# Kernel tuning notes

Measured on AMD Instinct MI355X. Metric: run time of the kernel, lower is better.

The kernel has to match this reference:

```python
import jax, jax.numpy as jnp
import numpy as np

N_NODES = 100000
N_EDGES = 1600000
F_IN = 256
F_HID = 128
BN_EPS = 1e-3


def setup_inputs() -> dict:
    key = jax.random.key(0)
    ks = jax.random.split(key, 10)
    x = jax.random.normal(ks[0], (N_NODES, F_IN), dtype=jnp.float32)
    edge_index = jax.random.randint(ks[1], (2, N_EDGES), 0, N_NODES, dtype=jnp.int64)
    edge_weight = jax.random.uniform(ks[2], (N_EDGES,), dtype=jnp.float32)
    # Layer 0: GCNConv 256 -> 128, Layer 1: GCNConv 128 -> 128
    W0 = jax.random.normal(ks[3], (F_IN, F_HID), dtype=jnp.float32) * (1.0 / np.sqrt(F_IN))
    b0 = jnp.zeros((F_HID,), dtype=jnp.float32)
    g0 = jnp.ones((F_HID,), dtype=jnp.float32)
    beta0 = jnp.zeros((F_HID,), dtype=jnp.float32)
    W1 = jax.random.normal(ks[4], (F_HID, F_HID), dtype=jnp.float32) * (1.0 / np.sqrt(F_HID))
    b1 = jnp.zeros((F_HID,), dtype=jnp.float32)
    g1 = jnp.ones((F_HID,), dtype=jnp.float32)
    beta1 = jnp.zeros((F_HID,), dtype=jnp.float32)
    return {"x": x, "edge_index": edge_index, "edge_weight": edge_weight,
            "W0": W0, "b0": b0, "g0": g0, "beta0": beta0,
            "W1": W1, "b1": b1, "g1": g1, "beta1": beta1}


def _gcn_conv(x, src, dst, ew, W, b):
    # PyG GCNConv: add self-loops (weight 1), symmetric normalization,
    # linear transform, scatter-aggregate over destination, then bias.
    h = x @ W                                            # [N, F_out]
    deg = jax.ops.segment_sum(ew, dst, num_segments=N_NODES) + 1.0  # +1 self-loop
    dinv = jnp.where(deg > 0, jax.lax.rsqrt(deg), 0.0)   # deg^{-1/2}
    norm = dinv[src] * ew * dinv[dst]                    # [E]
    agg = jax.ops.segment_sum(h[src] * norm[:, None], dst, num_segments=N_NODES)
    agg = agg + (dinv * dinv)[:, None] * h               # self-loop contribution
    return agg + b


def _batchnorm(x, gamma, beta):
    # training-mode BatchNorm1d math (batch stats, biased variance), eps=1e-3
    mu = jnp.mean(x, axis=0)
    var = jnp.mean(jnp.square(x - mu), axis=0)
    return (x - mu) * jax.lax.rsqrt(var + BN_EPS) * gamma + beta


def reference(x, edge_index, edge_weight, W0, b0, g0, beta0, W1, b1, g1, beta1):
    src, dst = edge_index[0], edge_index[1]
    # Layer 0: GCNConv -> BatchNorm -> ReLU -> Dropout(eval=identity)
    h = _gcn_conv(x, src, dst, edge_weight, W0, b0)
    h = jax.nn.relu(_batchnorm(h, g0, beta0))
    # Layer 1
    h = _gcn_conv(h, src, dst, edge_weight, W1, b1)
    h = jax.nn.relu(_batchnorm(h, g1, beta1))
    return h
```

## Files before the change

kernel.cpp:

```cpp
#include <hip/hip_runtime.h>
#include <stdint.h>

#define FIN 256
#define FHID 128
#define BN_EPS 1e-3f

#ifndef USE_GLL
#if defined(__has_builtin)
#if __has_builtin(__builtin_amdgcn_global_load_lds)
#define USE_GLL 1
#else
#define USE_GLL 0
#endif
#else
#define USE_GLL 0
#endif
#endif

typedef short bf16x8 __attribute__((ext_vector_type(8)));
typedef float f32x4 __attribute__((ext_vector_type(4)));

__device__ inline short f2bf(float f) {
    unsigned u = __float_as_uint(f);
    unsigned r = (u + 0x7FFFu + ((u >> 16) & 1u)) >> 16;
    return (short)r;
}
__device__ inline float bflo(unsigned v) { return __uint_as_float(v << 16); }
__device__ inline float bfhi(unsigned v) { return __uint_as_float(v & 0xFFFF0000u); }
__device__ inline float bf2f(short s) {
    return __uint_as_float(((unsigned)(unsigned short)s) << 16);
}

#define DEG_SCALE 131072.0f
#define DEG_INV   (1.0f / 131072.0f)

__global__ __launch_bounds__(256) void k_histprep(const int* __restrict__ ei, int E,
                                                  int HB, int CHUNKH, int nbuk,
                                                  unsigned* __restrict__ bcnt,
                                                  const float* __restrict__ W0,
                                                  const float* __restrict__ W1,
                                                  short* __restrict__ Wt0,
                                                  short* __restrict__ Wt1) {
    __shared__ unsigned hist[1024];
    if ((int)blockIdx.x < HB) {
        for (int i = threadIdx.x; i < nbuk; i += 256) hist[i] = 0;
        __syncthreads();
        const int e0 = blockIdx.x * CHUNKH;
        const int e1 = min(e0 + CHUNKH, E);
        for (int e = e0 + threadIdx.x; e < e1; e += 256)
            atomicAdd(&hist[ei[E + e] >> 7], 1u);
        __syncthreads();
        for (int k = threadIdx.x; k < nbuk; k += 256)
            bcnt[(size_t)blockIdx.x * nbuk + k] = hist[k];
    } else {
        int idx = ((int)blockIdx.x - HB) * 256 + threadIdx.x;
        if (idx < 32768) {
            int n = idx >> 8, k = idx & 255;
            Wt0[idx] = f2bf(W0[k * 128 + n]);
        } else {
            int j = idx - 32768;
            if (j < 16384) {
                int n = j >> 7, k = j & 127;
                Wt1[j] = f2bf(W1[k * 128 + n]);
            }
        }
    }
}

__device__ __forceinline__ void gemm0_body(int bid, float* xs,
                                           const float* __restrict__ X,
                                           const short* __restrict__ Wt,
                                           short* __restrict__ H, int nrows) {
    const int t = threadIdx.x;
    const int lane = t & 63;
    const int w = t >> 6;
    const int r0 = bid * 32;
    const int l15 = lane & 15;
    const int q = lane >> 4;

#pragma unroll
    for (int i = 0; i < 8; i++) {
        const int row = w * 8 + i;
        int grow = r0 + row; if (grow >= nrows) grow = nrows - 1;
        const char* gsrc = (const char*)(X + (size_t)grow * 256);
        const int swz = (row & 7) << 4;
#if USE_GLL
        __builtin_amdgcn_global_load_lds(gsrc + ((lane * 16) ^ swz),
                                         xs + row * 256, 16, 0, 0);
#else
        const float4 v = *reinterpret_cast<const float4*>(gsrc + ((lane * 16) ^ swz));
        *reinterpret_cast<float4*>((char*)xs + row * 1024 + lane * 16) = v;
#endif
    }
    __syncthreads();

    const int n0 = w * 32;
    const int swzr = (l15 & 7) << 4;

    f32x4 acc[2][2];
#pragma unroll
    for (int mf = 0; mf < 2; mf++)
#pragma unroll
        for (int nf = 0; nf < 2; nf++)
#pragma unroll
            for (int r = 0; r < 4; r++) acc[mf][nf][r] = 0.0f;

#pragma unroll
    for (int ks = 0; ks < 8; ks++) {
        const int cb = ks * 128 + q * 32;
        bf16x8 a[2];
#pragma unroll
        for (int mf = 0; mf < 2; mf++) {
            const char* rb = (const char*)xs + (size_t)(mf * 16 + l15) * 1024;
            const float4 u0 = *reinterpret_cast<const float4*>(rb + (cb ^ swzr));
            const float4 u1 = *reinterpret_cast<const float4*>(rb + ((cb + 16) ^ swzr));
            bf16x8 tt;
            tt[0] = f2bf(u0.x); tt[1] = f2bf(u0.y); tt[2] = f2bf(u0.z); tt[3] = f2bf(u0.w);
            tt[4] = f2bf(u1.x); tt[5] = f2bf(u1.y); tt[6] = f2bf(u1.z); tt[7] = f2bf(u1.w);
            a[mf] = tt;
        }
        const bf16x8 b0 = *reinterpret_cast<const bf16x8*>(
            Wt + (size_t)(n0 + l15) * 256 + ks * 32 + q * 8);
        const bf16x8 b1 = *reinterpret_cast<const bf16x8*>(
            Wt + (size_t)(n0 + 16 + l15) * 256 + ks * 32 + q * 8);
        acc[0][0] = __builtin_amdgcn_mfma_f32_16x16x32_bf16(a[0], b0, acc[0][0], 0, 0, 0);
        acc[1][0] = __builtin_amdgcn_mfma_f32_16x16x32_bf16(a[1], b0, acc[1][0], 0, 0, 0);
        acc[0][1] = __builtin_amdgcn_mfma_f32_16x16x32_bf16(a[0], b1, acc[0][1], 0, 0, 0);
        acc[1][1] = __builtin_amdgcn_mfma_f32_16x16x32_bf16(a[1], b1, acc[1][1], 0, 0, 0);
    }

#pragma unroll
    for (int mf = 0; mf < 2; mf++) {
        const int rbase = r0 + mf * 16 + (lane >> 4) * 4;
#pragma unroll
        for (int r = 0; r < 4; r++) {
            const int row = rbase + r;
            if (row < nrows) {
#pragma unroll
                for (int nf = 0; nf < 2; nf++)
                    H[(size_t)row * 128 + n0 + nf * 16 + l15] = f2bf(acc[mf][nf][r]);
            }
        }
    }
}

__global__ __launch_bounds__(256) void k_phaseCG(const int* __restrict__ ei,
                                                 const float* __restrict__ ew,
                                                 int E, int CHUNKC, int nbuk, int sub,
                                                 const unsigned* __restrict__ bcnt,
                                                 const unsigned* __restrict__ bbase,
                                                 int2* __restrict__ recs_mid,
                                                 int CBC,
                                                 const float* __restrict__ X,
                                                 const short* __restrict__ Wt,
                                                 short* __restrict__ H, int nrows) {
    __shared__ float xs[8192];
    if ((int)blockIdx.x < CBC) {
        unsigned* curs = (unsigned*)xs;
        const int b = blockIdx.x;
        for (int k = threadIdx.x; k < nbuk; k += 256)
            curs[k] = bbase[k] + bcnt[(size_t)(b * sub) * nbuk + k];
        __syncthreads();
        const int e0 = b * CHUNKC;
        const int e1 = min(e0 + CHUNKC, E);
        for (int base = e0; base < e1; base += 1024) {
            const int e = base + threadIdx.x * 4;
            if (e + 3 < e1) {
                const int4 s4 = *reinterpret_cast<const int4*>(ei + e);
                const int4 d4 = *reinterpret_cast<const int4*>(ei + E + e);
                const float4 w4 = *reinterpret_cast<const float4*>(ew + e);
                unsigned p0 = atomicAdd(&curs[d4.x >> 7], 1u);
                recs_mid[p0] = make_int2(s4.x | ((d4.x & 127) << 17), __float_as_int(w4.x));
                unsigned p1 = atomicAdd(&curs[d4.y >> 7], 1u);
                recs_mid[p1] = make_int2(s4.y | ((d4.y & 127) << 17), __float_as_int(w4.y));
                unsigned p2 = atomicAdd(&curs[d4.z >> 7], 1u);
                recs_mid[p2] = make_int2(s4.z | ((d4.z & 127) << 17), __float_as_int(w4.z));
                unsigned p3 = atomicAdd(&curs[d4.w >> 7], 1u);
                recs_mid[p3] = make_int2(s4.w | ((d4.w & 127) << 17), __float_as_int(w4.w));
            } else {
#pragma unroll
                for (int j = 0; j < 4; j++) {
                    const int ee = e + j;
                    if (ee < e1) {
                        int src = ei[ee];
                        int dst = ei[E + ee];
                        unsigned pos = atomicAdd(&curs[dst >> 7], 1u);
                        recs_mid[pos] = make_int2(src | ((dst & 127) << 17),
                                                  __float_as_int(ew[ee]));
                    }
                }
            }
        }
    } else {
        gemm0_body((int)blockIdx.x - CBC, xs, X, Wt, H, nrows);
    }
}

__global__ __launch_bounds__(256) void k_gemm1(const short* __restrict__ X,
                                               const short* __restrict__ Wt,
                                               const float* __restrict__ prm,
                                               short* __restrict__ H, int nrows) {
    __shared__ short xs[4096];
    const int t = threadIdx.x;
    const int lane = t & 63;
    const int w = t >> 6;
    const int r0 = blockIdx.x * 32;
    const int l15 = lane & 15;
    const int q = lane >> 4;

#pragma unroll
    for (int j = 0; j < 2; j++) {
        const int rbase = w * 8 + j * 4;
        const int row = rbase + q;
        int grow = r0 + row; if (grow >= nrows) grow = nrows - 1;
        const char* gsrc = (const char*)(X + (size_t)grow * 128);
        const int swz = (row & 7) << 4;
#if USE_GLL
        __builtin_amdgcn_global_load_lds(gsrc + (((lane & 15) * 16) ^ swz),
                                         xs + rbase * 128, 16, 0, 0);
#else
        const uint4 v = *reinterpret_cast<const uint4*>(gsrc + (((lane & 15) * 16) ^ swz));
        *reinterpret_cast<uint4*>((char*)xs + rbase * 256 + lane * 16) = v;
#endif
    }
    __syncthreads();

    const int n0 = w * 32;
    const int swzr = (l15 & 7) << 4;

    f32x4 acc[2][2];
#pragma unroll
    for (int mf = 0; mf < 2; mf++)
#pragma unroll
        for (int nf = 0; nf < 2; nf++)
#pragma unroll
            for (int r = 0; r < 4; r++) acc[mf][nf][r] = 0.0f;

#pragma unroll
    for (int ks = 0; ks < 4; ks++) {
        const int kb = ks * 32 + q * 8;
        const int cb = ks * 64 + q * 16;
        const float4 sc0 = *reinterpret_cast<const float4*>(prm + kb);
        const float4 sc1 = *reinterpret_cast<const float4*>(prm + kb + 4);
        const float4 sh0 = *reinterpret_cast<const float4*>(prm + 128 + kb);
        const float4 sh1 = *reinterpret_cast<const float4*>(prm + 128 + kb + 4);
        bf16x8 a[2];
#pragma unroll
        for (int mf = 0; mf < 2; mf++) {
            const char* rb = (const char*)xs + (size_t)(mf * 16 + l15) * 256;
            const bf16x8 ar = *reinterpret_cast<const bf16x8*>(rb + (cb ^ swzr));
            bf16x8 tt;
            tt[0] = f2bf(fmaxf(bf2f(ar[0]) * sc0.x + sh0.x, 0.f));
            tt[1] = f2bf(fmaxf(bf2f(ar[1]) * sc0.y + sh0.y, 0.f));
            tt[2] = f2bf(fmaxf(bf2f(ar[2]) * sc0.z + sh0.z, 0.f));
            tt[3] = f2bf(fmaxf(bf2f(ar[3]) * sc0.w + sh0.w, 0.f));
            tt[4] = f2bf(fmaxf(bf2f(ar[4]) * sc1.x + sh1.x, 0.f));
            tt[5] = f2bf(fmaxf(bf2f(ar[5]) * sc1.y + sh1.y, 0.f));
            tt[6] = f2bf(fmaxf(bf2f(ar[6]) * sc1.z + sh1.z, 0.f));
            tt[7] = f2bf(fmaxf(bf2f(ar[7]) * sc1.w + sh1.w, 0.f));
            a[mf] = tt;
        }
        const bf16x8 b0 = *reinterpret_cast<const bf16x8*>(
            Wt + (size_t)(n0 + l15) * 128 + kb);
        const bf16x8 b1 = *reinterpret_cast<const bf16x8*>(
            Wt + (size_t)(n0 + 16 + l15) * 128 + kb);
        acc[0][0] = __builtin_amdgcn_mfma_f32_16x16x32_bf16(a[0], b0, acc[0][0], 0, 0, 0);
        acc[1][0] = __builtin_amdgcn_mfma_f32_16x16x32_bf16(a[1], b0, acc[1][0], 0, 0, 0);
        acc[0][1] = __builtin_amdgcn_mfma_f32_16x16x32_bf16(a[0], b1, acc[0][1], 0, 0, 0);
        acc[1][1] = __builtin_amdgcn_mfma_f32_16x16x32_bf16(a[1], b1, acc[1][1], 0, 0, 0);
    }

#pragma unroll
    for (int mf = 0; mf < 2; mf++) {
        const int rbase = r0 + mf * 16 + (lane >> 4) * 4;
#pragma unroll
        for (int r = 0; r < 4; r++) {
            const int row = rbase + r;
            if (row < nrows) {
#pragma unroll
                for (int nf = 0; nf < 2; nf++)
                    H[(size_t)row * 128 + n0 + nf * 16 + l15] = f2bf(acc[mf][nf][r]);
            }
        }
    }
}

__global__ __launch_bounds__(256) void k_phaseB(unsigned* __restrict__ bcnt,
                                                unsigned* __restrict__ btotal,
                                                int HB, int nbuk) {
    __shared__ unsigned lds[256];
    const int k = blockIdx.x;
    const int t = threadIdx.x;
    unsigned v[4];
    unsigned s = 0;
#pragma unroll
    for (int i = 0; i < 4; i++) {
        int j = t * 4 + i;
        v[i] = (j < HB) ? bcnt[(size_t)j * nbuk + k] : 0;
        s += v[i];
    }
    lds[t] = s;
    __syncthreads();
    for (int off = 1; off < 256; off <<= 1) {
        unsigned add = (t >= off) ? lds[t - off] : 0;
        __syncthreads();
        lds[t] += add;
        __syncthreads();
    }
    unsigned run = lds[t] - s;
#pragma unroll
    for (int i = 0; i < 4; i++) {
        int j = t * 4 + i;
        if (j < HB) bcnt[(size_t)j * nbuk + k] = run;
        run += v[i];
    }
    if (t == 255) btotal[k] = lds[255];
}

__global__ __launch_bounds__(256) void k_bsum(const unsigned* __restrict__ btotal,
                                              unsigned* __restrict__ bbase,
                                              int nbuk, int E) {
    __shared__ unsigned lds[256];
    const int t = threadIdx.x;
    unsigned v[4];
    unsigned s = 0;
#pragma unroll
    for (int i = 0; i < 4; i++) {
        int j = t * 4 + i;
        v[i] = (j < nbuk) ? btotal[j] : 0;
        s += v[i];
    }
    lds[t] = s;
    __syncthreads();
    for (int off = 1; off < 256; off <<= 1) {
        unsigned add = (t >= off) ? lds[t - off] : 0;
        __syncthreads();
        lds[t] += add;
        __syncthreads();
    }
    unsigned run = lds[t] - s;
#pragma unroll
    for (int i = 0; i < 4; i++) {
        int j = t * 4 + i;
        if (j < nbuk) bbase[j] = run;
        run += v[i];
    }
    if (t == 255) bbase[nbuk] = (unsigned)E;
}

__global__ __launch_bounds__(256) void k_phaseD(const int2* __restrict__ recs_mid,
                                                const unsigned* __restrict__ bbase,
                                                float* __restrict__ dinv,
                                                int* __restrict__ rowptr,
                                                int2* __restrict__ recs,
                                                int n, int E) {
    __shared__ unsigned cnt[128], wsum[128], rank[128], sc[128], base[128];
    __shared__ float dloc[128];
    const int k = blockIdx.x;
    const int t = threadIdx.x;
    if (t < 128) { cnt[t] = 0; wsum[t] = 0; rank[t] = 0; }
    __syncthreads();
    const unsigned s0 = bbase[k], s1 = bbase[k + 1];
    for (unsigned i = s0 + t; i < s1; i += 256) {
        int2 r = recs_mid[i];
        int dl = (r.x >> 17) & 127;
        atomicAdd(&cnt[dl], 1u);
        atomicAdd(&wsum[dl], (unsigned)(__int_as_float(r.y) * DEG_SCALE));
    }
    __syncthreads();
    if (t < 128) sc[t] = cnt[t];
    __syncthreads();
    for (int off = 1; off < 128; off <<= 1) {
        unsigned add = (t < 128 && t >= off) ? sc[t - off] : 0;
        __syncthreads();
        if (t < 128) sc[t] += add;
        __syncthreads();
    }
    if (t < 128) {
        unsigned excl = sc[t] - cnt[t];
        base[t] = s0 + excl;
        int dst = k * 128 + t;
        if (dst < n) {
            float dg = (float)wsum[t] * DEG_INV + 1.0f;
            float dv = rsqrtf(dg);
            dloc[t] = dv;
            dinv[dst] = dv;
            rowptr[dst] = (int)(s0 + excl);
        }
    }
    if (k == 0 && t == 0) rowptr[n] = E;
    __syncthreads();
    for (unsigned i = s0 + t; i < s1; i += 256) {
        int2 r = recs_mid[i];
        int dl = (r.x >> 17) & 127;
        unsigned rr = atomicAdd(&rank[dl], 1u);
        float w2 = __int_as_float(r.y) * dloc[dl];
        recs[base[dl] + rr] = make_int2(r.x & 0x1FFFF, __float_as_int(w2));
    }
}

__global__ __launch_bounds__(256) void k_gather_stats(const short* __restrict__ h,
                                                      short* __restrict__ aggbf,
                                                      const int* __restrict__ rowptr,
                                                      const int2* __restrict__ recs,
                                                      const float* __restrict__ dinv,
                                                      const float* __restrict__ bias,
                                                      float* __restrict__ partial,
                                                      int n, int nstreams) {
    __shared__ float lsum[4][128], lsq[4][128];
    const int w = threadIdx.x >> 6;
    const int lane = threadIdx.x & 63;
    const int q3 = lane >> 4;
    const int f8 = (lane & 15) * 8;
    const float4 bv0 = *reinterpret_cast<const float4*>(bias + f8);
    const float4 bv1 = *reinterpret_cast<const float4*>(bias + f8 + 4);
    float s[8], qq[8];
#pragma unroll
    for (int j = 0; j < 8; j++) { s[j] = 0.f; qq[j] = 0.f; }

    for (int node = blockIdx.x * 16 + w * 4 + q3; node < n; node += nstreams) {
        float a[8];
#pragma unroll
        for (int j = 0; j < 8; j++) a[j] = 0.f;
        int e = rowptr[node];
        const int end = rowptr[node + 1];
        for (; e + 4 <= end; e += 4) {
            const int2 r0 = recs[e];
            const int2 r1 = recs[e + 1];
            const int2 r2 = recs[e + 2];
            const int2 r3 = recs[e + 3];
            const float d0 = dinv[r0.x];
            const float d1 = dinv[r1.x];
            const float d2 = dinv[r2.x];
            const float d3 = dinv[r3.x];
            const uint4 v0 = *reinterpret_cast<const uint4*>(h + (size_t)r0.x * 128 + f8);
            const uint4 v1 = *reinterpret_cast<const uint4*>(h + (size_t)r1.x * 128 + f8);
            const uint4 v2 = *reinterpret_cast<const uint4*>(h + (size_t)r2.x * 128 + f8);
            const uint4 v3 = *reinterpret_cast<const uint4*>(h + (size_t)r3.x * 128 + f8);
            const float w0 = __int_as_float(r0.y) * d0;
            const float w1 = __int_as_float(r1.y) * d1;
            const float w2 = __int_as_float(r2.y) * d2;
            const float w3 = __int_as_float(r3.y) * d3;
            a[0] += bflo(v0.x) * w0; a[1] += bfhi(v0.x) * w0;
            a[2] += bflo(v0.y) * w0; a[3] += bfhi(v0.y) * w0;
            a[4] += bflo(v0.z) * w0; a[5] += bfhi(v0.z) * w0;
            a[6] += bflo(v0.w) * w0; a[7] += bfhi(v0.w) * w0;
            a[0] += bflo(v1.x) * w1; a[1] += bfhi(v1.x) * w1;
            a[2] += bflo(v1.y) * w1; a[3] += bfhi(v1.y) * w1;
            a[4] += bflo(v1.z) * w1; a[5] += bfhi(v1.z) * w1;
            a[6] += bflo(v1.w) * w1; a[7] += bfhi(v1.w) * w1;
            a[0] += bflo(v2.x) * w2; a[1] += bfhi(v2.x) * w2;
            a[2] += bflo(v2.y) * w2; a[3] += bfhi(v2.y) * w2;
            a[4] += bflo(v2.z) * w2; a[5] += bfhi(v2.z) * w2;
            a[6] += bflo(v2.w) * w2; a[7] += bfhi(v2.w) * w2;
            a[0] += bflo(v3.x) * w3; a[1] += bfhi(v3.x) * w3;
            a[2] += bflo(v3.y) * w3; a[3] += bfhi(v3.y) * w3;
            a[4] += bflo(v3.z) * w3; a[5] += bfhi(v3.z) * w3;
            a[6] += bflo(v3.w) * w3; a[7] += bfhi(v3.w) * w3;
        }
        for (; e < end; e++) {
            const int2 r = recs[e];
            const float d = dinv[r.x];
            const uint4 v = *reinterpret_cast<const uint4*>(h + (size_t)r.x * 128 + f8);
            const float w0 = __int_as_float(r.y) * d;
            a[0] += bflo(v.x) * w0; a[1] += bfhi(v.x) * w0;
            a[2] += bflo(v.y) * w0; a[3] += bfhi(v.y) * w0;
            a[4] += bflo(v.z) * w0; a[5] += bfhi(v.z) * w0;
            a[6] += bflo(v.w) * w0; a[7] += bfhi(v.w) * w0;
        }
        const float di = dinv[node];
        const float sl = di * di;
        const uint4 hv = *reinterpret_cast<const uint4*>(h + (size_t)node * 128 + f8);
        float o[8];
        o[0] = a[0] + bflo(hv.x) * sl + bv0.x;
        o[1] = a[1] + bfhi(hv.x) * sl + bv0.y;
        o[2] = a[2] + bflo(hv.y) * sl + bv0.z;
        o[3] = a[3] + bfhi(hv.y) * sl + bv0.w;
        o[4] = a[4] + bflo(hv.z) * sl + bv1.x;
        o[5] = a[5] + bfhi(hv.z) * sl + bv1.y;
        o[6] = a[6] + bflo(hv.w) * sl + bv1.z;
        o[7] = a[7] + bfhi(hv.w) * sl + bv1.w;
        bf16x8 ob;
#pragma unroll
        for (int j = 0; j < 8; j++) ob[j] = f2bf(o[j]);
        *reinterpret_cast<bf16x8*>(aggbf + (size_t)node * 128 + f8) = ob;
#pragma unroll
        for (int j = 0; j < 8; j++) { s[j] += o[j]; qq[j] += o[j] * o[j]; }
    }

#pragma unroll
    for (int j = 0; j < 8; j++) {
        s[j] += __shfl_xor(s[j], 16);  s[j] += __shfl_xor(s[j], 32);
        qq[j] += __shfl_xor(qq[j], 16); qq[j] += __shfl_xor(qq[j], 32);
    }
    if (q3 == 0) {
        *reinterpret_cast<float4*>(&lsum[w][f8]) = make_float4(s[0], s[1], s[2], s[3]);
        *reinterpret_cast<float4*>(&lsum[w][f8 + 4]) = make_float4(s[4], s[5], s[6], s[7]);
        *reinterpret_cast<float4*>(&lsq[w][f8]) = make_float4(qq[0], qq[1], qq[2], qq[3]);
        *reinterpret_cast<float4*>(&lsq[w][f8 + 4]) = make_float4(qq[4], qq[5], qq[6], qq[7]);
    }
    __syncthreads();
    const int t = threadIdx.x;
    if (t < 128) {
        float ps = lsum[0][t] + lsum[1][t] + lsum[2][t] + lsum[3][t];
        float pq = lsq[0][t] + lsq[1][t] + lsq[2][t] + lsq[3][t];
        partial[(size_t)blockIdx.x * 256 + t] = ps;
        partial[(size_t)blockIdx.x * 256 + 128 + t] = pq;
    }
}

__global__ __launch_bounds__(256) void k_stats_bn(const float* __restrict__ partial,
                                                  const float* __restrict__ g,
                                                  const float* __restrict__ beta,
                                                  float* __restrict__ prm,
                                                  int nblk, int n) {
    __shared__ float wsm[4], wqm[4];
    const int f = blockIdx.x;
    const int t = threadIdx.x;
    const int per = nblk / 256;
    float s = 0.f, q = 0.f;
    for (int i = 0; i < per; i++) {
        int p = t * per + i;
        s += partial[(size_t)p * 256 + f];
        q += partial[(size_t)p * 256 + 128 + f];
    }
#pragma unroll
    for (int off = 1; off < 64; off <<= 1) {
        s += __shfl_xor(s, off);
        q += __shfl_xor(q, off);
    }
    if ((t & 63) == 0) { wsm[t >> 6] = s; wqm[t >> 6] = q; }
    __syncthreads();
    if (t == 0) {
        float S = wsm[0] + wsm[1] + wsm[2] + wsm[3];
        float Q = wqm[0] + wqm[1] + wqm[2] + wqm[3];
        float inv_n = 1.0f / (float)n;
        float mu = S * inv_n;
        float var = Q * inv_n - mu * mu;
        float sc = rsqrtf(var + BN_EPS) * g[f];
        prm[f] = sc;
        prm[128 + f] = beta[f] - mu * sc;
    }
}

__global__ __launch_bounds__(256) void k_bn_relu(const short* __restrict__ xbf,
                                                 float* __restrict__ y,
                                                 const float* __restrict__ prm, int n) {
    int idx = blockIdx.x * blockDim.x + threadIdx.x;
    const int total = n * 16;
    for (; idx < total; idx += gridDim.x * blockDim.x) {
        int node = idx >> 4;
        int f8 = (idx & 15) * 8;
        const uint4 v = *reinterpret_cast<const uint4*>(xbf + (size_t)node * 128 + f8);
        const float4 sc0 = *reinterpret_cast<const float4*>(prm + f8);
        const float4 sc1 = *reinterpret_cast<const float4*>(prm + f8 + 4);
        const float4 sh0 = *reinterpret_cast<const float4*>(prm + 128 + f8);
        const float4 sh1 = *reinterpret_cast<const float4*>(prm + 128 + f8 + 4);
        float4 o0, o1;
        o0.x = fmaxf(bflo(v.x) * sc0.x + sh0.x, 0.f);
        o0.y = fmaxf(bfhi(v.x) * sc0.y + sh0.y, 0.f);
        o0.z = fmaxf(bflo(v.y) * sc0.z + sh0.z, 0.f);
        o0.w = fmaxf(bfhi(v.y) * sc0.w + sh0.w, 0.f);
        o1.x = fmaxf(bflo(v.z) * sc1.x + sh1.x, 0.f);
        o1.y = fmaxf(bfhi(v.z) * sc1.y + sh1.y, 0.f);
        o1.z = fmaxf(bflo(v.w) * sc1.z + sh1.z, 0.f);
        o1.w = fmaxf(bfhi(v.w) * sc1.w + sh1.w, 0.f);
        float* yp = y + (size_t)node * 128 + f8;
        *reinterpret_cast<float4*>(yp) = o0;
        *reinterpret_cast<float4*>(yp + 4) = o1;
    }
}

extern "C" void kernel_launch(void* const* d_in, const int* in_sizes, int n_in,
                              void* d_out, int out_size, void* d_ws, size_t ws_size,
                              hipStream_t stream) {
    const float* x   = (const float*)d_in[0];
    const int*   ei  = (const int*)d_in[1];
    const float* ew  = (const float*)d_in[2];
    const float* W0  = (const float*)d_in[3];
    const float* b0  = (const float*)d_in[4];
    const float* g0  = (const float*)d_in[5];
    const float* be0 = (const float*)d_in[6];
    const float* W1  = (const float*)d_in[7];
    const float* b1  = (const float*)d_in[8];
    const float* g1  = (const float*)d_in[9];
    const float* be1 = (const float*)d_in[10];
    float* out = (float*)d_out;

    const int N = in_sizes[0] / FIN;
    const int E = in_sizes[2];
    const int NBUK = (N + 127) >> 7;
    const int HB = 1024;
    const int CHUNKH = (E + HB - 1) / HB;
    const int CBC = 256;
    const int SUB = HB / CBC;
    const int CHUNKC = CHUNKH * SUB;
    const int GB = 2048;

    short* aggbf    = (short*)d_ws;
    short* hbf      = aggbf + (size_t)N * 128;
    int2*  recs     = (int2*)(hbf + (size_t)N * 128);
    int2*  recs_mid = recs + E;
    unsigned* bcnt  = (unsigned*)(recs_mid + E);
    unsigned* btotal= bcnt + (size_t)HB * NBUK;
    unsigned* bbase = btotal + NBUK;
    float* dinv     = (float*)(bbase + NBUK + 1);
    int*   rowptr   = (int*)(dinv + N);
    float* prm      = (float*)(rowptr + N + 1);
    float* partial  = prm + 256;

    short* Wt0 = (short*)d_out;
    short* Wt1 = Wt0 + 256 * 128;

    const int gemm_blocks = (N + 31) / 32;

    k_histprep<<<HB + 192, 256, 0, stream>>>(ei, E, HB, CHUNKH, NBUK, bcnt,
                                             W0, W1, Wt0, Wt1);
    k_phaseB<<<NBUK, 256, 0, stream>>>(bcnt, btotal, HB, NBUK);
    k_bsum<<<1, 256, 0, stream>>>(btotal, bbase, NBUK, E);

    k_phaseCG<<<CBC + gemm_blocks, 256, 0, stream>>>(ei, ew, E, CHUNKC, NBUK, SUB,
                                                     bcnt, bbase, recs_mid, CBC,
                                                     x, Wt0, hbf, N);
    k_phaseD<<<NBUK, 256, 0, stream>>>(recs_mid, bbase, dinv, rowptr, recs, N, E);

    k_gather_stats<<<GB, 256, 0, stream>>>(hbf, aggbf, rowptr, recs, dinv, b0,
                                           partial, N, GB * 16);
    k_stats_bn<<<128, 256, 0, stream>>>(partial, g0, be0, prm, GB, N);

    k_gemm1<<<gemm_blocks, 256, 0, stream>>>(aggbf, Wt1, prm, hbf, N);
    k_gather_stats<<<GB, 256, 0, stream>>>(hbf, aggbf, rowptr, recs, dinv, b1,
                                           partial, N, GB * 16);
    k_stats_bn<<<128, 256, 0, stream>>>(partial, g1, be1, prm, GB, N);
    k_bn_relu<<<2048, 256, 0, stream>>>(aggbf, out, prm, N);
}
```

Measured before the change: 289.6 us.

## Use atomic work-stealing node scheduling and 8-way unroll in gather kernel

Replaces the static grid-stride assignment of 16-node groups in the gather/stats kernel with dynamic work distribution via a global atomic counter (one per layer, zeroed by a memset). The edge loop is also unrolled by 8 to keep more independent gathers in flight. The aim is to balance uneven per-node degrees across blocks and raise memory-level parallelism. In exchange it adds two __syncthreads and one atomic per 16 nodes, plus higher register pressure.

```diff
diff --git a/kernel.cpp b/kernel.cpp
--- a/kernel.cpp
+++ b/kernel.cpp
@@ -406,8 +406,10 @@
                                                       const float* __restrict__ dinv,
                                                       const float* __restrict__ bias,
                                                       float* __restrict__ partial,
-                                                      int n, int nstreams) {
+                                                      unsigned* __restrict__ ctr,
+                                                      int n) {
     __shared__ float lsum[4][128], lsq[4][128];
+    __shared__ int sh_base;
     const int w = threadIdx.x >> 6;
     const int lane = threadIdx.x & 63;
     const int q3 = lane >> 4;
@@ -418,74 +420,148 @@
 #pragma unroll
     for (int j = 0; j < 8; j++) { s[j] = 0.f; qq[j] = 0.f; }
 
-    for (int node = blockIdx.x * 16 + w * 4 + q3; node < n; node += nstreams) {
-        float a[8];
-#pragma unroll
-        for (int j = 0; j < 8; j++) a[j] = 0.f;
-        int e = rowptr[node];
-        const int end = rowptr[node + 1];
-        for (; e + 4 <= end; e += 4) {
-            const int2 r0 = recs[e];
-            const int2 r1 = recs[e + 1];
-            const int2 r2 = recs[e + 2];
-            const int2 r3 = recs[e + 3];
-            const float d0 = dinv[r0.x];
-            const float d1 = dinv[r1.x];
-            const float d2 = dinv[r2.x];
-            const float d3 = dinv[r3.x];
-            const uint4 v0 = *reinterpret_cast<const uint4*>(h + (size_t)r0.x * 128 + f8);
-            const uint4 v1 = *reinterpret_cast<const uint4*>(h + (size_t)r1.x * 128 + f8);
-            const uint4 v2 = *reinterpret_cast<const uint4*>(h + (size_t)r2.x * 128 + f8);
-            const uint4 v3 = *reinterpret_cast<const uint4*>(h + (size_t)r3.x * 128 + f8);
-            const float w0 = __int_as_float(r0.y) * d0;
-            const float w1 = __int_as_float(r1.y) * d1;
-            const float w2 = __int_as_float(r2.y) * d2;
-            const float w3 = __int_as_float(r3.y) * d3;
-            a[0] += bflo(v0.x) * w0; a[1] += bfhi(v0.x) * w0;
-            a[2] += bflo(v0.y) * w0; a[3] += bfhi(v0.y) * w0;
-            a[4] += bflo(v0.z) * w0; a[5] += bfhi(v0.z) * w0;
-            a[6] += bflo(v0.w) * w0; a[7] += bfhi(v0.w) * w0;
-            a[0] += bflo(v1.x) * w1; a[1] += bfhi(v1.x) * w1;
-            a[2] += bflo(v1.y) * w1; a[3] += bfhi(v1.y) * w1;
-            a[4] += bflo(v1.z) * w1; a[5] += bfhi(v1.z) * w1;
-            a[6] += bflo(v1.w) * w1; a[7] += bfhi(v1.w) * w1;
-            a[0] += bflo(v2.x) * w2; a[1] += bfhi(v2.x) * w2;
-            a[2] += bflo(v2.y) * w2; a[3] += bfhi(v2.y) * w2;
-            a[4] += bflo(v2.z) * w2; a[5] += bfhi(v2.z) * w2;
-            a[6] += bflo(v2.w) * w2; a[7] += bfhi(v2.w) * w2;
-            a[0] += bflo(v3.x) * w3; a[1] += bfhi(v3.x) * w3;
-            a[2] += bflo(v3.y) * w3; a[3] += bfhi(v3.y) * w3;
-            a[4] += bflo(v3.z) * w3; a[5] += bfhi(v3.z) * w3;
-            a[6] += bflo(v3.w) * w3; a[7] += bfhi(v3.w) * w3;
+    for (;;) {
+        __syncthreads();
+        if (threadIdx.x == 0) sh_base = (int)atomicAdd(ctr, 16u);
+        __syncthreads();
+        const int nb = sh_base;
+        if (nb >= n) break;
+        const int node = nb + w * 4 + q3;
+        if (node < n) {
+            float a[8];
+#pragma unroll
+            for (int j = 0; j < 8; j++) a[j] = 0.f;
+            int e = rowptr[node];
+            const int end = rowptr[node + 1];
+            for (; e + 8 <= end; e += 8) {
+                const int2 r0 = recs[e];
+                const int2 r1 = recs[e + 1];
+                const int2 r2 = recs[e + 2];
+                const int2 r3 = recs[e + 3];
+                const int2 r4 = recs[e + 4];
+                const int2 r5 = recs[e + 5];
+                const int2 r6 = recs[e + 6];
+                const int2 r7 = recs[e + 7];
+                const float d0 = dinv[r0.x];
+                const float d1 = dinv[r1.x];
+                const float d2 = dinv[r2.x];
+                const float d3 = dinv[r3.x];
+                const float d4 = dinv[r4.x];
+                const float d5 = dinv[r5.x];
+                const float d6 = dinv[r6.x];
+                const float d7 = dinv[r7.x];
+                const uint4 v0 = *reinterpret_cast<const uint4*>(h + (size_t)r0.x * 128 + f8);
+                const uint4 v1 = *reinterpret_cast<const uint4*>(h + (size_t)r1.x * 128 + f8);
+                const uint4 v2 = *reinterpret_cast<const uint4*>(h + (size_t)r2.x * 128 + f8);
+                const uint4 v3 = *reinterpret_cast<const uint4*>(h + (size_t)r3.x * 128 + f8);
+                const uint4 v4 = *reinterpret_cast<const uint4*>(h + (size_t)r4.x * 128 + f8);
+                const uint4 v5 = *reinterpret_cast<const uint4*>(h + (size_t)r5.x * 128 + f8);
+                const uint4 v6 = *reinterpret_cast<const uint4*>(h + (size_t)r6.x * 128 + f8);
+                const uint4 v7 = *reinterpret_cast<const uint4*>(h + (size_t)r7.x * 128 + f8);
+                const float w0 = __int_as_float(r0.y) * d0;
+                const float w1 = __int_as_float(r1.y) * d1;
+                const float w2 = __int_as_float(r2.y) * d2;
+                const float w3 = __int_as_float(r3.y) * d3;
+                const float w4 = __int_as_float(r4.y) * d4;
+                const float w5 = __int_as_float(r5.y) * d5;
+                const float w6 = __int_as_float(r6.y) * d6;
+                const float w7 = __int_as_float(r7.y) * d7;
+                a[0] += bflo(v0.x) * w0; a[1] += bfhi(v0.x) * w0;
+                a[2] += bflo(v0.y) * w0; a[3] += bfhi(v0.y) * w0;
+                a[4] += bflo(v0.z) * w0; a[5] += bfhi(v0.z) * w0;
+                a[6] += bflo(v0.w) * w0; a[7] += bfhi(v0.w) * w0;
+                a[0] += bflo(v1.x) * w1; a[1] += bfhi(v1.x) * w1;
+                a[2] += bflo(v1.y) * w1; a[3] += bfhi(v1.y) * w1;
+                a[4] += bflo(v1.z) * w1; a[5] += bfhi(v1.z) * w1;
+                a[6] += bflo(v1.w) * w1; a[7] += bfhi(v1.w) * w1;
+                a[0] += bflo(v2.x) * w2; a[1] += bfhi(v2.x) * w2;
+                a[2] += bflo(v2.y) * w2; a[3] += bfhi(v2.y) * w2;
+                a[4] += bflo(v2.z) * w2; a[5] += bfhi(v2.z) * w2;
+                a[6] += bflo(v2.w) * w2; a[7] += bfhi(v2.w) * w2;
+                a[0] += bflo(v3.x) * w3; a[1] += bfhi(v3.x) * w3;
+                a[2] += bflo(v3.y) * w3; a[3] += bfhi(v3.y) * w3;
+                a[4] += bflo(v3.z) * w3; a[5] += bfhi(v3.z) * w3;
+                a[6] += bflo(v3.w) * w3; a[7] += bfhi(v3.w) * w3;
+                a[0] += bflo(v4.x) * w4; a[1] += bfhi(v4.x) * w4;
+                a[2] += bflo(v4.y) * w4; a[3] += bfhi(v4.y) * w4;
+                a[4] += bflo(v4.z) * w4; a[5] += bfhi(v4.z) * w4;
+                a[6] += bflo(v4.w) * w4; a[7] += bfhi(v4.w) * w4;
+                a[0] += bflo(v5.x) * w5; a[1] += bfhi(v5.x) * w5;
+                a[2] += bflo(v5.y) * w5; a[3] += bfhi(v5.y) * w5;
+                a[4] += bflo(v5.z) * w5; a[5] += bfhi(v5.z) * w5;
+                a[6] += bflo(v5.w) * w5; a[7] += bfhi(v5.w) * w5;
+                a[0] += bflo(v6.x) * w6; a[1] += bfhi(v6.x) * w6;
+                a[2] += bflo(v6.y) * w6; a[3] += bfhi(v6.y) * w6;
+                a[4] += bflo(v6.z) * w6; a[5] += bfhi(v6.z) * w6;
+                a[6] += bflo(v6.w) * w6; a[7] += bfhi(v6.w) * w6;
+                a[0] += bflo(v7.x) * w7; a[1] += bfhi(v7.x) * w7;
+                a[2] += bflo(v7.y) * w7; a[3] += bfhi(v7.y) * w7;
+                a[4] += bflo(v7.z) * w7; a[5] += bfhi(v7.z) * w7;
+                a[6] += bflo(v7.w) * w7; a[7] += bfhi(v7.w) * w7;
+            }
+            for (; e + 4 <= end; e += 4) {
+                const int2 r0 = recs[e];
+                const int2 r1 = recs[e + 1];
+                const int2 r2 = recs[e + 2];
+                const int2 r3 = recs[e + 3];
+                const float d0 = dinv[r0.x];
+                const float d1 = dinv[r1.x];
+                const float d2 = dinv[r2.x];
+                const float d3 = dinv[r3.x];
+                const uint4 v0 = *reinterpret_cast<const uint4*>(h + (size_t)r0.x * 128 + f8);
+                const uint4 v1 = *reinterpret_cast<const uint4*>(h + (size_t)r1.x * 128 + f8);
+                const uint4 v2 = *reinterpret_cast<const uint4*>(h + (size_t)r2.x * 128 + f8);
+                const uint4 v3 = *reinterpret_cast<const uint4*>(h + (size_t)r3.x * 128 + f8);
+                const float w0 = __int_as_float(r0.y) * d0;
+                const float w1 = __int_as_float(r1.y) * d1;
+                const float w2 = __int_as_float(r2.y) * d2;
+                const float w3 = __int_as_float(r3.y) * d3;
+                a[0] += bflo(v0.x) * w0; a[1] += bfhi(v0.x) * w0;
+                a[2] += bflo(v0.y) * w0; a[3] += bfhi(v0.y) * w0;
+                a[4] += bflo(v0.z) * w0; a[5] += bfhi(v0.z) * w0;
+                a[6] += bflo(v0.w) * w0; a[7] += bfhi(v0.w) * w0;
+                a[0] += bflo(v1.x) * w1; a[1] += bfhi(v1.x) * w1;
+                a[2] += bflo(v1.y) * w1; a[3] += bfhi(v1.y) * w1;
+                a[4] += bflo(v1.z) * w1; a[5] += bfhi(v1.z) * w1;
+                a[6] += bflo(v1.w) * w1; a[7] += bfhi(v1.w) * w1;
+                a[0] += bflo(v2.x) * w2; a[1] += bfhi(v2.x) * w2;
+                a[2] += bflo(v2.y) * w2; a[3] += bfhi(v2.y) * w2;
+                a[4] += bflo(v2.z) * w2; a[5] += bfhi(v2.z) * w2;
+                a[6] += bflo(v2.w) * w2; a[7] += bfhi(v2.w) * w2;
+                a[0] += bflo(v3.x) * w3; a[1] += bfhi(v3.x) * w3;
+                a[2] += bflo(v3.y) * w3; a[3] += bfhi(v3.y) * w3;
+                a[4] += bflo(v3.z) * w3; a[5] += bfhi(v3.z) * w3;
+                a[6] += bflo(v3.w) * w3; a[7] += bfhi(v3.w) * w3;
+            }
+            for (; e < end; e++) {
+                const int2 r = recs[e];
+                const float d = dinv[r.x];
+                const uint4 v = *reinterpret_cast<const uint4*>(h + (size_t)r.x * 128 + f8);
+                const float w0 = __int_as_float(r.y) * d;
+                a[0] += bflo(v.x) * w0; a[1] += bfhi(v.x) * w0;
+                a[2] += bflo(v.y) * w0; a[3] += bfhi(v.y) * w0;
+                a[4] += bflo(v.z) * w0; a[5] += bfhi(v.z) * w0;
+                a[6] += bflo(v.w) * w0; a[7] += bfhi(v.w) * w0;
+            }
+            const float di = dinv[node];
+            const float sl = di * di;
+            const uint4 hv = *reinterpret_cast<const uint4*>(h + (size_t)node * 128 + f8);
+            float o[8];
+            o[0] = a[0] + bflo(hv.x) * sl + bv0.x;
+            o[1] = a[1] + bfhi(hv.x) * sl + bv0.y;
+            o[2] = a[2] + bflo(hv.y) * sl + bv0.z;
+            o[3] = a[3] + bfhi(hv.y) * sl + bv0.w;
+            o[4] = a[4] + bflo(hv.z) * sl + bv1.x;
+            o[5] = a[5] + bfhi(hv.z) * sl + bv1.y;
+            o[6] = a[6] + bflo(hv.w) * sl + bv1.z;
+            o[7] = a[7] + bfhi(hv.w) * sl + bv1.w;
+            bf16x8 ob;
+#pragma unroll
+            for (int j = 0; j < 8; j++) ob[j] = f2bf(o[j]);
+            *reinterpret_cast<bf16x8*>(aggbf + (size_t)node * 128 + f8) = ob;
+#pragma unroll
+            for (int j = 0; j < 8; j++) { s[j] += o[j]; qq[j] += o[j] * o[j]; }
         }
-        for (; e < end; e++) {
-            const int2 r = recs[e];
-            const float d = dinv[r.x];
-            const uint4 v = *reinterpret_cast<const uint4*>(h + (size_t)r.x * 128 + f8);
-            const float w0 = __int_as_float(r.y) * d;
-            a[0] += bflo(v.x) * w0; a[1] += bfhi(v.x) * w0;
-            a[2] += bflo(v.y) * w0; a[3] += bfhi(v.y) * w0;
-            a[4] += bflo(v.z) * w0; a[5] += bfhi(v.z) * w0;
-            a[6] += bflo(v.w) * w0; a[7] += bfhi(v.w) * w0;
-        }
-        const float di = dinv[node];
-        const float sl = di * di;
-        const uint4 hv = *reinterpret_cast<const uint4*>(h + (size_t)node * 128 + f8);
-        float o[8];
-        o[0] = a[0] + bflo(hv.x) * sl + bv0.x;
-        o[1] = a[1] + bfhi(hv.x) * sl + bv0.y;
-        o[2] = a[2] + bflo(hv.y) * sl + bv0.z;
-        o[3] = a[3] + bfhi(hv.y) * sl + bv0.w;
-        o[4] = a[4] + bflo(hv.z) * sl + bv1.x;
-        o[5] = a[5] + bfhi(hv.z) * sl + bv1.y;
-        o[6] = a[6] + bflo(hv.w) * sl + bv1.z;
-        o[7] = a[7] + bfhi(hv.w) * sl + bv1.w;
-        bf16x8 ob;
-#pragma unroll
-        for (int j = 0; j < 8; j++) ob[j] = f2bf(o[j]);
-        *reinterpret_cast<bf16x8*>(aggbf + (size_t)node * 128 + f8) = ob;
-#pragma unroll
-        for (int j = 0; j < 8; j++) { s[j] += o[j]; qq[j] += o[j] * o[j]; }
     }
 
 #pragma unroll
@@ -606,7 +682,8 @@
     unsigned* bbase = btotal + NBUK;
     float* dinv     = (float*)(bbase + NBUK + 1);
     int*   rowptr   = (int*)(dinv + N);
-    float* prm      = (float*)(rowptr + N + 1);
+    unsigned* ctr   = (unsigned*)(rowptr + N + 1);
+    float* prm      = (float*)(ctr + 2);
     float* partial  = prm + 256;
 
     short* Wt0 = (short*)d_out;
@@ -614,6 +691,7 @@
 
     const int gemm_blocks = (N + 31) / 32;
 
+    hipMemsetAsync(ctr, 0, 8, stream);
     k_histprep<<<HB + 192, 256, 0, stream>>>(ei, E, HB, CHUNKH, NBUK, bcnt,
                                              W0, W1, Wt0, Wt1);
     k_phaseB<<<NBUK, 256, 0, stream>>>(bcnt, btotal, HB, NBUK);
@@ -625,12 +703,12 @@
     k_phaseD<<<NBUK, 256, 0, stream>>>(recs_mid, bbase, dinv, rowptr, recs, N, E);
 
     k_gather_stats<<<GB, 256, 0, stream>>>(hbf, aggbf, rowptr, recs, dinv, b0,
-                                           partial, N, GB * 16);
+                                           partial, ctr, N);
     k_stats_bn<<<128, 256, 0, stream>>>(partial, g0, be0, prm, GB, N);
 
     k_gemm1<<<gemm_blocks, 256, 0, stream>>>(aggbf, Wt1, prm, hbf, N);
     k_gather_stats<<<GB, 256, 0, stream>>>(hbf, aggbf, rowptr, recs, dinv, b1,
-                                           partial, N, GB * 16);
+                                           partial, ctr + 1, N);
     k_stats_bn<<<128, 256, 0, stream>>>(partial, g1, be1, prm, GB, N);
     k_bn_relu<<<2048, 256, 0, stream>>>(aggbf, out, prm, N);
 }
```

New measurement: 380.3 us. 1.31x slower.
